# Performance work log

Measured on AMD Instinct MI355X. Metric: run time of the kernel, lower is better.

Reference implementation:

```python
import jax, jax.numpy as jnp
import numpy as np

N_NODES = 296960   # 1024 graphs x 290 padded nodes
N_EDGES = 2375680  # avg degree 8
BATCH = 1024
IN_FEATS = 75
DIM = 128
N_LAYERS = 3


def setup_inputs() -> dict:
    key = jax.random.key(0)
    ks = jax.random.split(key, 8)
    node_feats = jax.random.normal(ks[0], (N_NODES, IN_FEATS), dtype=jnp.float32)
    src = jax.random.randint(ks[1], (N_EDGES,), 0, N_NODES, dtype=jnp.int32)
    dst = jax.random.randint(ks[2], (N_EDGES,), 0, N_NODES, dtype=jnp.int32)
    # init_transform: Linear(75 -> 128, bias=False)
    W_init = jax.random.normal(ks[3], (IN_FEATS, DIM), dtype=jnp.float32) * 0.1
    # per-layer GraphConv weight/bias and residual Linear weight/bias (stacked over layers)
    W_gc = jax.random.normal(ks[4], (N_LAYERS, DIM, DIM), dtype=jnp.float32) * 0.05
    b_gc = jnp.zeros((N_LAYERS, DIM), dtype=jnp.float32)
    W_res = jax.random.normal(ks[5], (N_LAYERS, DIM, DIM), dtype=jnp.float32) * 0.05
    b_res = jnp.zeros((N_LAYERS, DIM), dtype=jnp.float32)
    return dict(node_feats=node_feats, src=src, dst=dst, W_init=W_init,
                W_gc=W_gc, b_gc=b_gc, W_res=W_res, b_res=b_res)


def reference(node_feats, src, dst, W_init, W_gc, b_gc, W_res, b_res):
    # MolecularGCN.forward: init_transform (no bias) -> 3 GCN layers -> reshape to (B, max_nodes, D)
    h = node_feats @ W_init  # [N, 128]
    for l in range(N_LAYERS):
        # GraphConv with norm='none': plain neighbor-sum aggregation (copy_u + sum),
        # then dense transform + bias + relu (in_feats == out_feats -> aggregate first).
        agg = jax.ops.segment_sum(h[src], dst, num_segments=N_NODES)  # [N, 128]
        new_feats = jax.nn.relu(agg @ W_gc[l] + b_gc[l])
        # GCNLayer residual branch: activation(res_connection(feats))
        res_feats = jax.nn.relu(h @ W_res[l] + b_res[l])
        h = new_feats + res_feats
    return h.reshape(BATCH, -1, DIM)  # [1024, 290, 128]
```

## Files before the change

### kernel.cpp

```cpp
#include <hip/hip_runtime.h>

#define N_NODES 296960
#define N_EDGES 2375680
#define IN_FEATS 75
#define DIM 128
#define N_LAYERS 3
#define ECAP 4096
#define KPAD 104
#define KUSE 96
#define NCHUNK 128
#define CHN (N_NODES / NCHUNK)
#define ETILE 2048
#define EBLKS (N_EDGES / ETILE)
#define CVPT 5

static_assert(N_NODES % 256 == 0, "node count divisible by 256");
static_assert(N_EDGES % ETILE == 0, "edge count divisible by tile");
static_assert(NCHUNK * CHN == N_NODES, "chunks cover nodes exactly");

typedef __attribute__((ext_vector_type(8))) short s8v;
typedef __attribute__((ext_vector_type(4))) float f4v;

__device__ __forceinline__ float u2f(unsigned int x) {
    union { unsigned int u; float f; } v; v.u = x; return v.f;
}
__device__ __forceinline__ unsigned short f2b(float f) {
    union { float f; unsigned int u; } v; v.f = f;
    unsigned int r = v.u + 0x7fffu + ((v.u >> 16) & 1u);
    return (unsigned short)(r >> 16);
}
__device__ __forceinline__ void addbf(f4v& a, uint2 q) {
    a.x += u2f(q.x << 16);
    a.y += u2f(q.x & 0xffff0000u);
    a.z += u2f(q.y << 16);
    a.w += u2f(q.y & 0xffff0000u);
}

__global__ void zero_i(int* __restrict__ p, int n) {
    int i = blockIdx.x * blockDim.x + threadIdx.x;
    if (i < n) p[i] = 0;
}

__global__ __launch_bounds__(256) void coarse_hist(const int* __restrict__ dst,
                                                   int* __restrict__ ccnt) {
    __shared__ int cnt[NCHUNK];
    const int tid = threadIdx.x;
    if (tid < NCHUNK) cnt[tid] = 0;
    __syncthreads();
    const int base = blockIdx.x * ETILE;
    #pragma unroll
    for (int i = 0; i < ETILE / 256; ++i) {
        const int d = dst[base + i * 256 + tid];
        atomicAdd(&cnt[d / CHN], 1);
    }
    __syncthreads();
    if (tid < NCHUNK && cnt[tid] > 0) atomicAdd(&ccnt[tid], cnt[tid]);
}

__global__ void coarse_scan(const int* __restrict__ ccnt, int* __restrict__ bucketBase) {
    __shared__ int lds[NCHUNK];
    const int tid = threadIdx.x;
    if (tid < NCHUNK) lds[tid] = ccnt[tid];
    __syncthreads();
    if (tid == 0) {
        int run = 0;
        for (int k = 0; k < NCHUNK; ++k) {
            const int v = lds[k];
            lds[k] = run;
            run += v;
        }
        bucketBase[NCHUNK] = run;
    }
    __syncthreads();
    if (tid < NCHUNK) bucketBase[tid] = lds[tid];
}

__global__ __launch_bounds__(256) void bucket_pass(
    const int* __restrict__ src, const int* __restrict__ dst,
    const int* __restrict__ bucketBase, int* __restrict__ bcur,
    unsigned int* __restrict__ bedge) {
    __shared__ int cnt[NCHUNK];
    __shared__ int cnt2[NCHUNK];
    __shared__ int basei[NCHUNK];
    const int tid = threadIdx.x;
    if (tid < NCHUNK) { cnt[tid] = 0; cnt2[tid] = 0; }
    __syncthreads();

    const int base = blockIdx.x * ETILE;
    int s8[ETILE / 256], b8[ETILE / 256], dl8[ETILE / 256];
    #pragma unroll
    for (int i = 0; i < ETILE / 256; ++i) {
        const int e = base + i * 256 + tid;
        s8[i] = src[e];
        const int d = dst[e];
        b8[i] = d / CHN;
        dl8[i] = d - b8[i] * CHN;
        atomicAdd(&cnt[b8[i]], 1);
    }
    __syncthreads();
    if (tid < NCHUNK && cnt[tid] > 0)
        basei[tid] = bucketBase[tid] + atomicAdd(&bcur[tid], cnt[tid]);
    __syncthreads();
    #pragma unroll
    for (int i = 0; i < ETILE / 256; ++i) {
        const int pos = basei[b8[i]] + atomicAdd(&cnt2[b8[i]], 1);
        bedge[pos] = ((unsigned int)dl8[i] << 19) | (unsigned int)s8[i];
    }
}

__global__ __launch_bounds__(512) void csr_pass(
    const unsigned int* __restrict__ bedge, const int* __restrict__ bucketBase,
    int* __restrict__ rowptr, int* __restrict__ eidx) {
    __shared__ int cnt[512 * CVPT];
    __shared__ int wexcl[9];
    const int tid = threadIdx.x;
    const int c = blockIdx.x;
    const int nodeBase = c * CHN;
    const int segBeg = bucketBase[c];
    const int nseg = bucketBase[c + 1] - segBeg;

    #pragma unroll
    for (int j = 0; j < CVPT; ++j) cnt[tid * CVPT + j] = 0;
    __syncthreads();

    for (int i = tid; i < nseg; i += 512)
        atomicAdd(&cnt[bedge[segBeg + i] >> 19], 1);
    __syncthreads();

    int v[CVPT];
    int s = 0;
    #pragma unroll
    for (int j = 0; j < CVPT; ++j) { v[j] = cnt[tid * CVPT + j]; s += v[j]; }
    const int lane = tid & 63, wid = tid >> 6;
    int x = s;
    #pragma unroll
    for (int st = 1; st < 64; st <<= 1) {
        const int t = __shfl_up(x, st, 64);
        if (lane >= st) x += t;
    }
    if (lane == 63) wexcl[wid + 1] = x;
    __syncthreads();
    if (tid == 0) {
        wexcl[0] = 0;
        for (int k = 1; k <= 8; ++k) wexcl[k] += wexcl[k - 1];
    }
    __syncthreads();
    int run = segBeg + wexcl[wid] + (x - s);
    #pragma unroll
    for (int j = 0; j < CVPT; ++j) { cnt[tid * CVPT + j] = run; run += v[j]; }
    __syncthreads();

    for (int n = tid; n < CHN; n += 512)
        rowptr[nodeBase + n] = cnt[n];
    if (c == NCHUNK - 1 && tid == 0) rowptr[N_NODES] = N_EDGES;
    __syncthreads();

    for (int i = tid; i < nseg; i += 512) {
        const unsigned int p = bedge[segBeg + i];
        const int pos = atomicAdd(&cnt[p >> 19], 1);
        eidx[pos] = (int)(p & 0x7FFFFu);
    }
}

__global__ void wcvt(const float* __restrict__ Wgc, const float* __restrict__ Wres,
                     unsigned short* __restrict__ Wt) {
    const int m = blockIdx.x >> 6;
    const int idx = (blockIdx.x & 63) * 256 + threadIdx.x;
    const float* src = (m < 3) ? (Wgc + m * 16384) : (Wres + (m - 3) * 16384);
    const int n = idx >> 7, k = idx & 127;
    Wt[m * 16384 + idx] = f2b(src[k * 128 + n]);
}

__global__ void wcvt_init(const float* __restrict__ Wi, unsigned short* __restrict__ WtI) {
    int idx = blockIdx.x * 256 + threadIdx.x;
    if (idx >= 128 * KUSE) return;
    int n = idx / KUSE, k = idx - n * KUSE;
    WtI[idx] = (k < IN_FEATS) ? f2b(Wi[(size_t)k * DIM + n]) : (unsigned short)0;
}

__global__ __launch_bounds__(256) void init_mfma(const float* __restrict__ X,
                                                 const unsigned short* __restrict__ WtI,
                                                 unsigned short* __restrict__ H) {
    __shared__ short sX[32][KPAD];
    const int tid = threadIdx.x;
    const int rowBase = blockIdx.x * 32;

    for (int idx = tid; idx < 32 * IN_FEATS; idx += 256) {
        const int row = idx / IN_FEATS;
        const int k = idx - row * IN_FEATS;
        sX[row][k] = (short)f2b(X[(size_t)rowBase * IN_FEATS + idx]);
    }
    #pragma unroll
    for (int i = 0; i < 4; ++i) {
        const int idx = tid + i * 256;
        const int row = idx >> 5;
        const int col = IN_FEATS + (idx & 31);
        if (col < KPAD) sX[row][col] = 0;
    }
    __syncthreads();

    const int w = tid >> 6;
    const int l = tid & 63;
    const int lr = l & 15;
    const int lk = l >> 4;

    f4v acc[2][2] = {{{0.f,0.f,0.f,0.f},{0.f,0.f,0.f,0.f}},{{0.f,0.f,0.f,0.f},{0.f,0.f,0.f,0.f}}};

    #pragma unroll
    for (int kb = 0; kb < 3; ++kb) {
        const int kofs = kb * 32 + lk * 8;
        s8v a[2], b[2];
        a[0] = *reinterpret_cast<const s8v*>(&sX[lr][kofs]);
        a[1] = *reinterpret_cast<const s8v*>(&sX[16 + lr][kofs]);
        #pragma unroll
        for (int ct = 0; ct < 2; ++ct) {
            const int col = w * 32 + ct * 16 + lr;
            b[ct] = *reinterpret_cast<const s8v*>(WtI + (size_t)col * KUSE + kofs);
        }
        #pragma unroll
        for (int rt = 0; rt < 2; ++rt)
            #pragma unroll
            for (int ct = 0; ct < 2; ++ct)
                acc[rt][ct] = __builtin_amdgcn_mfma_f32_16x16x32_bf16(a[rt], b[ct], acc[rt][ct], 0, 0, 0);
    }

    #pragma unroll
    for (int ct = 0; ct < 2; ++ct) {
        const int col = w * 32 + ct * 16 + lr;
        #pragma unroll
        for (int rt = 0; rt < 2; ++rt)
            #pragma unroll
            for (int r = 0; r < 4; ++r) {
                const int row = rowBase + rt * 16 + lk * 4 + r;
                H[(size_t)row * DIM + col] = f2b(acc[rt][ct][r]);
            }
    }
}

template <int LAST>
__global__ __launch_bounds__(256) void layer_mfma(
    const unsigned short* __restrict__ Hin, unsigned short* __restrict__ HoutB,
    float* __restrict__ HoutF,
    const int* __restrict__ rowptr, const int* __restrict__ eidx,
    const unsigned short* __restrict__ WgcT, const unsigned short* __restrict__ WresT,
    const float* __restrict__ bgc, const float* __restrict__ bres) {
    __shared__ short sTiles[2][32][DIM];
    int* sE = (int*)&sTiles[0][0][0];
    char* aggB = (char*)&sTiles[0][0][0];
    char* ownB = (char*)&sTiles[1][0][0];

    const int tid = threadIdx.x;
    const int rowBase = blockIdx.x * 32;

    const int blkBeg = rowptr[rowBase];
    const int blkEnd = rowptr[rowBase + 32];
    const int nE = blkEnd - blkBeg;
    const int nStage = (nE < ECAP) ? nE : ECAP;

    for (int i = tid; i < nStage; i += 256)
        sE[i] = eidx[blkBeg + i];
    __syncthreads();

    const int g = tid >> 5;
    const int lane = tid & 31;
    const unsigned short* HinL = Hin + lane * 4;

    int begv[4], endv[4], rel[4];
    f4v acc[4];
    uint2 own[4];
    int md = 0;
    #pragma unroll
    for (int ii = 0; ii < 4; ++ii) {
        const int node = rowBase + g * 4 + ii;
        begv[ii] = rowptr[node];
        endv[ii] = rowptr[node + 1];
        rel[ii] = begv[ii] - blkBeg;
        own[ii] = *reinterpret_cast<const uint2*>(HinL + (size_t)node * DIM);
        acc[ii] = (f4v){0.f, 0.f, 0.f, 0.f};
        const int d = endv[ii] - begv[ii];
        md = (d > md) ? d : md;
    }

    if (nE <= ECAP) {
        for (int t = 0; t < md; t += 2) {
            #pragma unroll
            for (int ii = 0; ii < 4; ++ii) {
                const int ea = begv[ii] + t;
                const int eb = ea + 1;
                uint2 qa = make_uint2(0u, 0u), qb = make_uint2(0u, 0u);
                if (ea < endv[ii])
                    qa = *reinterpret_cast<const uint2*>(HinL + (size_t)sE[rel[ii] + t] * DIM);
                if (eb < endv[ii])
                    qb = *reinterpret_cast<const uint2*>(HinL + (size_t)sE[rel[ii] + t + 1] * DIM);
                addbf(acc[ii], qa);
                addbf(acc[ii], qb);
            }
        }
    } else {
        #pragma unroll
        for (int ii = 0; ii < 4; ++ii) {
            for (int e = begv[ii]; e < endv[ii]; ++e) {
                const int s = eidx[e];
                addbf(acc[ii], *reinterpret_cast<const uint2*>(HinL + (size_t)s * DIM));
            }
        }
    }
    __syncthreads();

    #pragma unroll
    for (int ii = 0; ii < 4; ++ii) {
        const int row = g * 4 + ii;
        const int kbyte = lane * 8;
        const int sw = kbyte ^ ((row & 7) << 4);
        uint2 p;
        p.x = (unsigned)f2b(acc[ii].x) | ((unsigned)f2b(acc[ii].y) << 16);
        p.y = (unsigned)f2b(acc[ii].z) | ((unsigned)f2b(acc[ii].w) << 16);
        *reinterpret_cast<uint2*>(aggB + row * 256 + sw) = p;
        *reinterpret_cast<uint2*>(ownB + row * 256 + sw) = own[ii];
    }
    __syncthreads();

    const int w = tid >> 6;
    const int l = tid & 63;
    const int lr = l & 15;
    const int lk = l >> 4;

    f4v accG[2][2] = {{{0.f,0.f,0.f,0.f},{0.f,0.f,0.f,0.f}},{{0.f,0.f,0.f,0.f},{0.f,0.f,0.f,0.f}}};
    f4v accR[2][2] = {{{0.f,0.f,0.f,0.f},{0.f,0.f,0.f,0.f}},{{0.f,0.f,0.f,0.f},{0.f,0.f,0.f,0.f}}};

    #pragma unroll
    for (int kb = 0; kb < 4; ++kb) {
        const int kofs = kb * 32 + lk * 8;
        const int kbyte = kofs * 2;
        s8v aG[2], aO[2];
        #pragma unroll
        for (int rt = 0; rt < 2; ++rt) {
            const int row = rt * 16 + lr;
            const int byte = row * 256 + (kbyte ^ ((row & 7) << 4));
            aG[rt] = *reinterpret_cast<const s8v*>(aggB + byte);
            aO[rt] = *reinterpret_cast<const s8v*>(ownB + byte);
        }
        s8v bG[2], bR[2];
        #pragma unroll
        for (int ct = 0; ct < 2; ++ct) {
            const int col = w * 32 + ct * 16 + lr;
            const size_t off = (size_t)col * DIM + kofs;
            bG[ct] = *reinterpret_cast<const s8v*>(WgcT + off);
            bR[ct] = *reinterpret_cast<const s8v*>(WresT + off);
        }
        #pragma unroll
        for (int rt = 0; rt < 2; ++rt) {
            #pragma unroll
            for (int ct = 0; ct < 2; ++ct) {
                accG[rt][ct] = __builtin_amdgcn_mfma_f32_16x16x32_bf16(aG[rt], bG[ct], accG[rt][ct], 0, 0, 0);
                accR[rt][ct] = __builtin_amdgcn_mfma_f32_16x16x32_bf16(aO[rt], bR[ct], accR[rt][ct], 0, 0, 0);
            }
        }
    }

    #pragma unroll
    for (int ct = 0; ct < 2; ++ct) {
        const int col = w * 32 + ct * 16 + lr;
        const float bg = bgc[col];
        const float br = bres[col];
        #pragma unroll
        for (int rt = 0; rt < 2; ++rt) {
            #pragma unroll
            for (int r = 0; r < 4; ++r) {
                const int row = rowBase + rt * 16 + lk * 4 + r;
                const float v = fmaxf(accG[rt][ct][r] + bg, 0.f) + fmaxf(accR[rt][ct][r] + br, 0.f);
                if (LAST) HoutF[(size_t)row * DIM + col] = v;
                else      HoutB[(size_t)row * DIM + col] = f2b(v);
            }
        }
    }
}

__global__ void init_mm(const float* __restrict__ X, const float* __restrict__ W,
                        float* __restrict__ H) {
    __shared__ float sF[8 * IN_FEATS];
    const int tid = threadIdx.x;
    const long rowBase = (long)blockIdx.x * 8;
    for (int i = tid; i < 8 * IN_FEATS; i += 256)
        sF[i] = X[rowBase * IN_FEATS + i];
    __syncthreads();
    const int r = tid >> 5;
    const int c = (tid & 31) * 4;
    float4 acc = make_float4(0.f, 0.f, 0.f, 0.f);
    for (int k = 0; k < IN_FEATS; ++k) {
        const float a = sF[r * IN_FEATS + k];
        const float4 w = *reinterpret_cast<const float4*>(W + k * DIM + c);
        acc.x += a * w.x; acc.y += a * w.y; acc.z += a * w.z; acc.w += a * w.w;
    }
    *reinterpret_cast<float4*>(H + (rowBase + r) * DIM + c) = acc;
}

__global__ void zero_f4(float4* __restrict__ p, int n4) {
    int i = blockIdx.x * blockDim.x + threadIdx.x;
    if (i < n4) p[i] = make_float4(0.f, 0.f, 0.f, 0.f);
}

__global__ void scatter_add(const float* __restrict__ H, const int* __restrict__ src,
                            const int* __restrict__ dst, float* __restrict__ agg) {
    const long t = (long)blockIdx.x * blockDim.x + threadIdx.x;
    const int e = (int)(t >> 5);
    const int lane = (int)(t & 31);
    if (e >= N_EDGES) return;
    const int s = src[e];
    const int d = dst[e];
    const float4 v = *reinterpret_cast<const float4*>(H + (long)s * DIM + lane * 4);
    float* o = agg + (long)d * DIM + lane * 4;
    unsafeAtomicAdd(o + 0, v.x);
    unsafeAtomicAdd(o + 1, v.y);
    unsafeAtomicAdd(o + 2, v.z);
    unsafeAtomicAdd(o + 3, v.w);
}

__global__ void layer_mm(const float* __restrict__ agg, float* __restrict__ H,
                         const float* __restrict__ Wgc, const float* __restrict__ bgc,
                         const float* __restrict__ Wres, const float* __restrict__ bres) {
    __shared__ float sA[8][DIM];
    __shared__ float sH[8][DIM];
    const int tid = threadIdx.x;
    const long rowBase = (long)blockIdx.x * 8;
    const int r = tid >> 5;
    const int c = (tid & 31) * 4;
    *reinterpret_cast<float4*>(&sA[r][c]) =
        *reinterpret_cast<const float4*>(agg + (rowBase + r) * DIM + c);
    *reinterpret_cast<float4*>(&sH[r][c]) =
        *reinterpret_cast<const float4*>(H + (rowBase + r) * DIM + c);
    __syncthreads();
    float4 a1 = make_float4(0.f, 0.f, 0.f, 0.f);
    float4 a2 = make_float4(0.f, 0.f, 0.f, 0.f);
    #pragma unroll 8
    for (int k = 0; k < DIM; ++k) {
        const float av = sA[r][k];
        const float hv = sH[r][k];
        const float4 wg = *reinterpret_cast<const float4*>(Wgc + k * DIM + c);
        const float4 wr = *reinterpret_cast<const float4*>(Wres + k * DIM + c);
        a1.x += av * wg.x; a1.y += av * wg.y; a1.z += av * wg.z; a1.w += av * wg.w;
        a2.x += hv * wr.x; a2.y += hv * wr.y; a2.z += hv * wr.z; a2.w += hv * wr.w;
    }
    const float4 bg = *reinterpret_cast<const float4*>(bgc + c);
    const float4 br = *reinterpret_cast<const float4*>(bres + c);
    float4 o;
    o.x = fmaxf(a1.x + bg.x, 0.f) + fmaxf(a2.x + br.x, 0.f);
    o.y = fmaxf(a1.y + bg.y, 0.f) + fmaxf(a2.y + br.y, 0.f);
    o.z = fmaxf(a1.z + bg.z, 0.f) + fmaxf(a2.z + br.z, 0.f);
    o.w = fmaxf(a1.w + bg.w, 0.f) + fmaxf(a2.w + br.w, 0.f);
    *reinterpret_cast<float4*>(H + (rowBase + r) * DIM + c) = o;
}

extern "C" void kernel_launch(void* const* d_in, const int* in_sizes, int n_in,
                              void* d_out, int out_size, void* d_ws, size_t ws_size,
                              hipStream_t stream) {
    const float* node_feats = (const float*)d_in[0];
    const int*   src        = (const int*)d_in[1];
    const int*   dst        = (const int*)d_in[2];
    const float* W_init     = (const float*)d_in[3];
    const float* W_gc       = (const float*)d_in[4];
    const float* b_gc       = (const float*)d_in[5];
    const float* W_res      = (const float*)d_in[6];
    const float* b_res      = (const float*)d_in[7];

    const size_t HB_BYTES  = (size_t)N_NODES * DIM * sizeof(unsigned short);
    const size_t RP_BYTES  = ((size_t)(N_NODES + 1) * 4 + 255) & ~255ull;
    const size_t DEG_BYTES = ((size_t)N_NODES * 4 + 255) & ~255ull;
    const size_t CUR_BYTES = DEG_BYTES;
    const size_t BS_BYTES  = (((size_t)(N_NODES / 256)) * 4 + 255) & ~255ull;
    const size_t EIDX_BYTES = (size_t)N_EDGES * 4;
    const size_t NEED = 2 * HB_BYTES + RP_BYTES + DEG_BYTES + CUR_BYTES + BS_BYTES + EIDX_BYTES;

    if (ws_size >= NEED) {
        char* w = (char*)d_ws;
        unsigned short* Ha = (unsigned short*)w;      w += HB_BYTES;
        unsigned short* Hb = (unsigned short*)w;      w += HB_BYTES;
        int* rowptr = (int*)w;                        w += RP_BYTES;
        int* small  = (int*)w;                        w += DEG_BYTES;
        int* wtarea = (int*)w;                        w += CUR_BYTES;
        w += BS_BYTES;
        int* eidx   = (int*)w;

        int* ccnt       = small;
        int* bcur       = small + NCHUNK;
        int* bucketBase = small + 2 * NCHUNK;
        unsigned int* bedge = (unsigned int*)Hb;
        unsigned short* Wt  = (unsigned short*)wtarea;
        unsigned short* WtI = Wt + 6 * 16384;
        float* Hout = (float*)d_out;

        zero_i<<<1, 256, 0, stream>>>(small, 2 * NCHUNK);
        coarse_hist<<<EBLKS, 256, 0, stream>>>(dst, ccnt);
        coarse_scan<<<1, NCHUNK, 0, stream>>>(ccnt, bucketBase);
        bucket_pass<<<EBLKS, 256, 0, stream>>>(src, dst, bucketBase, bcur, bedge);
        csr_pass<<<NCHUNK, 512, 0, stream>>>(bedge, bucketBase, rowptr, eidx);

        wcvt<<<6 * 64, 256, 0, stream>>>(W_gc, W_res, Wt);
        wcvt_init<<<(128 * KUSE + 255) / 256, 256, 0, stream>>>(W_init, WtI);
        init_mfma<<<N_NODES / 32, 256, 0, stream>>>(node_feats, WtI, Ha);

        layer_mfma<0><<<N_NODES / 32, 256, 0, stream>>>(
            Ha, Hb, nullptr, rowptr, eidx, Wt + 0 * 16384, Wt + 3 * 16384, b_gc, b_res);
        layer_mfma<0><<<N_NODES / 32, 256, 0, stream>>>(
            Hb, Ha, nullptr, rowptr, eidx, Wt + 1 * 16384, Wt + 4 * 16384,
            b_gc + DIM, b_res + DIM);
        layer_mfma<1><<<N_NODES / 32, 256, 0, stream>>>(
            Ha, nullptr, Hout, rowptr, eidx, Wt + 2 * 16384, Wt + 5 * 16384,
            b_gc + 2 * DIM, b_res + 2 * DIM);
    } else {
        float* H   = (float*)d_out;
        float* agg = (float*)d_ws;
        const int n4 = N_NODES * DIM / 4;
        init_mm<<<N_NODES / 8, 256, 0, stream>>>(node_feats, W_init, H);
        for (int l = 0; l < N_LAYERS; ++l) {
            zero_f4<<<(n4 + 255) / 256, 256, 0, stream>>>((float4*)agg, n4);
            scatter_add<<<(N_EDGES * 32) / 256, 256, 0, stream>>>(H, src, dst, agg);
            layer_mm<<<N_NODES / 8, 256, 0, stream>>>(agg, H,
                W_gc + (size_t)l * DIM * DIM, b_gc + (size_t)l * DIM,
                W_res + (size_t)l * DIM * DIM, b_res + (size_t)l * DIM);
        }
    }
}
```

Measured before the change: 615.4 us.

## Widen gather loads to 16-byte rows and stage bf16 output through LDS

The neighbor-gather phase now assigns 16 lanes per node, with each lane loading 8 bf16 values (uint4), and it unrolls edges by 4 so more loads are in flight. Previously 32 lanes each loaded 4 values, two edges at a time. For non-final layers, the bf16 outputs are first written to shared memory and then stored to global memory as coalesced 16-byte rows, replacing scattered 2-byte stores. The aim is fewer, wider memory transactions in both the gather and the store. The cost is two extra barriers and higher register pressure from the unrolled loads.

```diff
diff --git a/kernel.cpp b/kernel.cpp
--- a/kernel.cpp
+++ b/kernel.cpp
@@ -29,11 +29,11 @@
     unsigned int r = v.u + 0x7fffu + ((v.u >> 16) & 1u);
     return (unsigned short)(r >> 16);
 }
-__device__ __forceinline__ void addbf(f4v& a, uint2 q) {
-    a.x += u2f(q.x << 16);
-    a.y += u2f(q.x & 0xffff0000u);
-    a.z += u2f(q.y << 16);
-    a.w += u2f(q.y & 0xffff0000u);
+__device__ __forceinline__ void addbf8(f4v& a, f4v& b, uint4 q) {
+    a.x += u2f(q.x << 16); a.y += u2f(q.x & 0xffff0000u);
+    a.z += u2f(q.y << 16); a.w += u2f(q.y & 0xffff0000u);
+    b.x += u2f(q.z << 16); b.y += u2f(q.z & 0xffff0000u);
+    b.z += u2f(q.w << 16); b.w += u2f(q.w & 0xffff0000u);
 }
 
 __global__ void zero_i(int* __restrict__ p, int n) {
@@ -261,62 +261,67 @@
         sE[i] = eidx[blkBeg + i];
     __syncthreads();
 
-    const int g = tid >> 5;
-    const int lane = tid & 31;
-    const unsigned short* HinL = Hin + lane * 4;
-
-    int begv[4], endv[4], rel[4];
-    f4v acc[4];
-    uint2 own[4];
+    const int gg = tid >> 4;
+    const int lane16 = tid & 15;
+    const unsigned short* HinL = Hin + lane16 * 8;
+
+    int begv[2], endv[2], rel[2];
+    f4v accA[2], accB[2];
+    uint4 own[2];
     int md = 0;
     #pragma unroll
-    for (int ii = 0; ii < 4; ++ii) {
-        const int node = rowBase + g * 4 + ii;
+    for (int ii = 0; ii < 2; ++ii) {
+        const int node = rowBase + gg * 2 + ii;
         begv[ii] = rowptr[node];
         endv[ii] = rowptr[node + 1];
         rel[ii] = begv[ii] - blkBeg;
-        own[ii] = *reinterpret_cast<const uint2*>(HinL + (size_t)node * DIM);
-        acc[ii] = (f4v){0.f, 0.f, 0.f, 0.f};
+        own[ii] = *reinterpret_cast<const uint4*>(HinL + (size_t)node * DIM);
+        accA[ii] = (f4v){0.f, 0.f, 0.f, 0.f};
+        accB[ii] = (f4v){0.f, 0.f, 0.f, 0.f};
         const int d = endv[ii] - begv[ii];
         md = (d > md) ? d : md;
     }
 
     if (nE <= ECAP) {
-        for (int t = 0; t < md; t += 2) {
-            #pragma unroll
-            for (int ii = 0; ii < 4; ++ii) {
-                const int ea = begv[ii] + t;
-                const int eb = ea + 1;
-                uint2 qa = make_uint2(0u, 0u), qb = make_uint2(0u, 0u);
-                if (ea < endv[ii])
-                    qa = *reinterpret_cast<const uint2*>(HinL + (size_t)sE[rel[ii] + t] * DIM);
-                if (eb < endv[ii])
-                    qb = *reinterpret_cast<const uint2*>(HinL + (size_t)sE[rel[ii] + t + 1] * DIM);
-                addbf(acc[ii], qa);
-                addbf(acc[ii], qb);
-            }
+        for (int t = 0; t < md; t += 4) {
+            uint4 q[2][4];
+            #pragma unroll
+            for (int ii = 0; ii < 2; ++ii)
+                #pragma unroll
+                for (int j = 0; j < 4; ++j) {
+                    q[ii][j] = make_uint4(0u, 0u, 0u, 0u);
+                    const int e = begv[ii] + t + j;
+                    if (e < endv[ii])
+                        q[ii][j] = *reinterpret_cast<const uint4*>(
+                            HinL + (size_t)sE[rel[ii] + t + j] * DIM);
+                }
+            #pragma unroll
+            for (int ii = 0; ii < 2; ++ii)
+                #pragma unroll
+                for (int j = 0; j < 4; ++j)
+                    addbf8(accA[ii], accB[ii], q[ii][j]);
         }
     } else {
         #pragma unroll
-        for (int ii = 0; ii < 4; ++ii) {
-            for (int e = begv[ii]; e < endv[ii]; ++e) {
-                const int s = eidx[e];
-                addbf(acc[ii], *reinterpret_cast<const uint2*>(HinL + (size_t)s * DIM));
-            }
-        }
-    }
-    __syncthreads();
-
-    #pragma unroll
-    for (int ii = 0; ii < 4; ++ii) {
-        const int row = g * 4 + ii;
-        const int kbyte = lane * 8;
+        for (int ii = 0; ii < 2; ++ii)
+            for (int e = begv[ii]; e < endv[ii]; ++e)
+                addbf8(accA[ii], accB[ii],
+                       *reinterpret_cast<const uint4*>(HinL + (size_t)eidx[e] * DIM));
+    }
+    __syncthreads();
+
+    #pragma unroll
+    for (int ii = 0; ii < 2; ++ii) {
+        const int row = gg * 2 + ii;
+        const int kbyte = lane16 * 16;
         const int sw = kbyte ^ ((row & 7) << 4);
-        uint2 p;
-        p.x = (unsigned)f2b(acc[ii].x) | ((unsigned)f2b(acc[ii].y) << 16);
-        p.y = (unsigned)f2b(acc[ii].z) | ((unsigned)f2b(acc[ii].w) << 16);
-        *reinterpret_cast<uint2*>(aggB + row * 256 + sw) = p;
-        *reinterpret_cast<uint2*>(ownB + row * 256 + sw) = own[ii];
+        uint4 p;
+        p.x = (unsigned)f2b(accA[ii].x) | ((unsigned)f2b(accA[ii].y) << 16);
+        p.y = (unsigned)f2b(accA[ii].z) | ((unsigned)f2b(accA[ii].w) << 16);
+        p.z = (unsigned)f2b(accB[ii].x) | ((unsigned)f2b(accB[ii].y) << 16);
+        p.w = (unsigned)f2b(accB[ii].z) | ((unsigned)f2b(accB[ii].w) << 16);
+        *reinterpret_cast<uint4*>(aggB + row * 256 + sw) = p;
+        *reinterpret_cast<uint4*>(ownB + row * 256 + sw) = own[ii];
     }
     __syncthreads();
 
@@ -358,20 +363,46 @@
         }
     }
 
-    #pragma unroll
-    for (int ct = 0; ct < 2; ++ct) {
-        const int col = w * 32 + ct * 16 + lr;
-        const float bg = bgc[col];
-        const float br = bres[col];
-        #pragma unroll
-        for (int rt = 0; rt < 2; ++rt) {
-            #pragma unroll
-            for (int r = 0; r < 4; ++r) {
-                const int row = rowBase + rt * 16 + lk * 4 + r;
-                const float v = fmaxf(accG[rt][ct][r] + bg, 0.f) + fmaxf(accR[rt][ct][r] + br, 0.f);
-                if (LAST) HoutF[(size_t)row * DIM + col] = v;
-                else      HoutB[(size_t)row * DIM + col] = f2b(v);
-            }
+    if (LAST) {
+        #pragma unroll
+        for (int ct = 0; ct < 2; ++ct) {
+            const int col = w * 32 + ct * 16 + lr;
+            const float bg = bgc[col];
+            const float br = bres[col];
+            #pragma unroll
+            for (int rt = 0; rt < 2; ++rt)
+                #pragma unroll
+                for (int r = 0; r < 4; ++r) {
+                    const int row = rowBase + rt * 16 + lk * 4 + r;
+                    HoutF[(size_t)row * DIM + col] =
+                        fmaxf(accG[rt][ct][r] + bg, 0.f) + fmaxf(accR[rt][ct][r] + br, 0.f);
+                }
+        }
+    } else {
+        __syncthreads();
+        short* eOut = (short*)aggB;
+        #pragma unroll
+        for (int ct = 0; ct < 2; ++ct) {
+            const int col = w * 32 + ct * 16 + lr;
+            const float bg = bgc[col];
+            const float br = bres[col];
+            #pragma unroll
+            for (int rt = 0; rt < 2; ++rt)
+                #pragma unroll
+                for (int r = 0; r < 4; ++r) {
+                    const int row = rt * 16 + lk * 4 + r;
+                    eOut[row * DIM + col] = (short)f2b(
+                        fmaxf(accG[rt][ct][r] + bg, 0.f) + fmaxf(accR[rt][ct][r] + br, 0.f));
+                }
+        }
+        __syncthreads();
+        #pragma unroll
+        for (int i = 0; i < 2; ++i) {
+            const int id = tid + i * 256;
+            const int row = id >> 4;
+            const int col8 = (id & 15) * 8;
+            *reinterpret_cast<uint4*>(HoutB + (size_t)(rowBase + row) * DIM + col8) =
+                *reinterpret_cast<const uint4*>(eOut + row * DIM + col8);
         }
     }
 }
```

Measured after the change: 608.6 us. Within noise of the previous version (-1.1%).
